# Performance work log

Measured on AMD Instinct MI355X. Metric: run time of the kernel, lower is better.

The kernel has to match this reference:

```python
import jax, jax.numpy as jnp
import numpy as np

N_HEAD = 12
D_MODEL = 768
B, T = 1, 1024


def _rope(x):
    # x: (B, H, T, Dh). Matches torch RoPE: split even/odd, cat halves.
    Dh = x.shape[-1]
    t = x.shape[2]
    inv_freq = 1.0 / (10000.0 ** (jnp.arange(0, Dh, 2, dtype=jnp.float32) / Dh))
    freqs = jnp.arange(t, dtype=jnp.float32)[:, None] * inv_freq[None, :]  # (T, Dh/2)
    cos = jnp.cos(freqs)[None, None]  # (1,1,T,Dh/2)
    sin = jnp.sin(freqs)[None, None]
    x1 = x[..., 0::2]
    x2 = x[..., 1::2]
    return jnp.concatenate([-x2 * sin + x1 * cos, x1 * sin + x2 * cos], axis=-1)


def _wedge(x, A, id_bias):
    # S = (A - A^T) + diag(id_bias_h), per head h; x: (B,H,T,Dh)
    skew = A - A.T  # (Dh, Dh)
    S = skew[None, :, :] + jax.vmap(jnp.diag)(id_bias)  # (H, Dh, Dh)
    flow = jnp.einsum('bhtd,hde->bhte', x, S)
    return x + flow


def _forward(x, WV_w, WV_b, WK_w, WK_b, WQ_w, A, id_bias, sink, v_nulls, WO_w, WO_b):
    b, t, c = x.shape
    n_br = WO_w.shape[0]
    n_sh = n_br
    dh = c // n_br
    h_tot = n_br * n_sh
    scale = dh ** -0.5

    q = (x @ WQ_w).reshape(b, t, h_tot, dh).transpose(0, 2, 1, 3)      # (B,Htot,T,Dh)
    k_base = (x @ WK_w + WK_b).reshape(b, t, n_sh, dh).transpose(0, 2, 1, 3)
    v_base = (x @ WV_w + WV_b).reshape(b, t, n_sh, dh).transpose(0, 2, 1, 3)
    k = jnp.tile(k_base, (1, n_br, 1, 1))  # (B,Htot,T,Dh)
    v = jnp.tile(v_base, (1, n_br, 1, 1))

    q = _rope(_wedge(q, A, id_bias))
    k = _rope(_wedge(k, A, id_bias))

    scores = jnp.einsum('bhtd,bhsd->bhts', q, k) * scale  # (B,Htot,T,T)
    causal = jnp.tril(jnp.ones((t, t), dtype=bool))
    scores = jnp.where(causal[None, None], scores, -jnp.inf)

    sinks = jnp.broadcast_to(sink.reshape(1, h_tot, 1, 1), (b, h_tot, t, 1))
    probs = jax.nn.softmax(jnp.concatenate([scores, sinks], axis=-1), axis=-1)
    probs_tok, probs_sink = probs[..., :t], probs[..., t:]

    out_tok = jnp.einsum('bhts,bhsd->bhtd', probs_tok, v)
    out_sink = probs_sink * v_nulls.reshape(h_tot, dh)[None, :, None, :]
    ctx = out_tok + out_sink  # (B,Htot,T,Dh)

    ctx = ctx.reshape(b, n_br, n_sh, t, dh).transpose(0, 1, 3, 2, 4).reshape(b, n_br, t, c)
    y = jnp.einsum('bntc,ncd->bntd', ctx, WO_w) + WO_b[None, :, None, :]
    return y.mean(axis=1)  # (B,T,C)


def setup_inputs() -> dict:
    key = jax.random.key(0)
    ks = jax.random.split(key, 12)
    c = D_MODEL
    n_br = N_HEAD
    dh = c // n_br
    h_tot = n_br * n_br
    s = 0.02
    return {
        'x': jax.random.normal(ks[0], (B, T, c), dtype=jnp.float32),
        'WV_w': jax.random.normal(ks[1], (c, c), dtype=jnp.float32) * s,
        'WV_b': jnp.zeros((c,), dtype=jnp.float32),
        'WK_w': jax.random.normal(ks[2], (c, c), dtype=jnp.float32) * s,
        'WK_b': jnp.zeros((c,), dtype=jnp.float32),
        'WQ_w': jax.random.normal(ks[3], (c, c * n_br), dtype=jnp.float32) * s,
        'A': jax.random.normal(ks[4], (dh, dh), dtype=jnp.float32) * s,
        'id_bias': jax.random.normal(ks[5], (h_tot, dh), dtype=jnp.float32) * s,
        'sink': jax.random.normal(ks[6], (h_tot,), dtype=jnp.float32) * s,
        'v_nulls': jax.random.normal(ks[7], (n_br, c), dtype=jnp.float32) * s,
        'WO_w': jax.random.normal(ks[8], (n_br, c, c), dtype=jnp.float32) * (1.0 / np.sqrt(c)),
        'WO_b': jnp.zeros((n_br, c), dtype=jnp.float32),
    }


def reference(x, WV_w, WV_b, WK_w, WK_b, WQ_w, A, id_bias, sink, v_nulls, WO_w, WO_b):
    return _forward(x, WV_w, WV_b, WK_w, WK_b, WQ_w, A, id_bias, sink, v_nulls, WO_w, WO_b)
```

## Files before the change

### kernel.cpp

```cpp
#include <hip/hip_runtime.h>
#include <hip/hip_bf16.h>

#define T_SEQ   1024
#define C_MODEL 768
#define N_BR    12
#define DH      64
#define H_TOT   144
#define NQ      9216

typedef __bf16 bf16x8 __attribute__((ext_vector_type(8)));
typedef float  f32x4  __attribute__((ext_vector_type(4)));
typedef unsigned int u32x4 __attribute__((ext_vector_type(4)));
typedef unsigned short u16;

#define SM_OFF 3.0f
#define LOG2E  1.44269504089f
#define QSCALE (0.125f * LOG2E)

__device__ __forceinline__ void gload16(void* lds, const void* g)
{
    __builtin_amdgcn_global_load_lds(
        (const __attribute__((address_space(1))) void*)g,
        (__attribute__((address_space(3))) void*)lds, 16, 0, 0);
}

__device__ __forceinline__ void split1(float x, u16& h, u16& l)
{
    __bf16 bh = (__bf16)x;
    __bf16 bl = (__bf16)(x - (float)bh);
    h = __builtin_bit_cast(u16, bh);
    l = __builtin_bit_cast(u16, bl);
}

__device__ __forceinline__ u16 tobf(float x)
{
    return __builtin_bit_cast(u16, (__bf16)x);
}

__device__ __forceinline__ unsigned cvtpk(float a, float b)
{
    unsigned r;
    asm("v_cvt_pk_bf16_f32 %0, %1, %2" : "=v"(r) : "v"(a), "v"(b));
    return r;
}

__device__ __forceinline__ float exp2raw(float x)
{
    float r;
    asm("v_exp_f32 %0, %1" : "=v"(r) : "v"(x));
    return r;
}

__device__ __forceinline__ int swb(int row, int byteoff)
{
    return row * 128 + (byteoff ^ ((row & 7) << 4));
}

__device__ __forceinline__ bf16x8 ldsr8(const u16* p, int byteoff)
{
    return *reinterpret_cast<const bf16x8*>(reinterpret_cast<const char*>(p) + byteoff);
}

__device__ __forceinline__ void convt_body(const float* __restrict__ W,
                                           u16* __restrict__ out, int K, int N,
                                           int nx, int ky, float (*t)[33], int tid)
{
    const int n0 = nx * 32;
    const int k0 = ky * 32;
    const int tx = tid & 31;
    const int ty = tid >> 5;
    #pragma unroll
    for (int r = 0; r < 4; ++r)
        t[ty + r * 8][tx] = W[(size_t)(k0 + ty + r * 8) * N + n0 + tx];
    __syncthreads();
    #pragma unroll
    for (int r = 0; r < 4; ++r)
        out[(size_t)(n0 + ty + r * 8) * K + k0 + tx] = tobf(t[tx][ty + r * 8]);
}

__global__ __launch_bounds__(256)
void prep_kernel(const float* __restrict__ x, u16* __restrict__ xh,
                 const float* __restrict__ Amat, const float* __restrict__ id_bias,
                 u16* __restrict__ Mth, u16* __restrict__ Mtl,
                 const float* __restrict__ WO_b, float* __restrict__ mbias,
                 float* __restrict__ tab,
                 const float* __restrict__ WO_w, u16* __restrict__ wot,
                 const float* __restrict__ WK_w, const float* __restrict__ WV_w,
                 u16* __restrict__ wkvt)
{
    __shared__ float tsh[32][33];
    const int b   = blockIdx.x;
    const int tid = threadIdx.x;

    if (b < 128) {
        const int idx = b * 256 + tid;
        const int t = idx >> 5, i = idx & 31;
        const float inv = expf(-(float)i * (logf(10000.f) / 32.f));
        const float fr = (float)t * inv;
        tab[t * 64 + i]      = cosf(fr);
        tab[t * 64 + 32 + i] = sinf(fr);
    } else if (b < 272) {
        const int h = b - 128;
        const int base = tid * 16;
        #pragma unroll
        for (int i = 0; i < 16; ++i) {
            const int idx = base + i;
            const int e = idx >> 6, d = idx & 63;
            float v = Amat[d * 64 + e] - Amat[e * 64 + d];
            if (d == e) v += 1.0f + id_bias[h * 64 + d];
            u16 hh, ll;
            split1(v, hh, ll);
            Mth[(size_t)h * 4096 + idx] = hh;
            Mtl[(size_t)h * 4096 + idx] = ll;
        }
    } else if (b < 275) {
        const int d = (b - 272) * 256 + tid;
        if (d < C_MODEL) {
            float s = 0.f;
            #pragma unroll
            for (int n = 0; n < N_BR; ++n) s += WO_b[n * C_MODEL + d];
            mbias[d] = s * (1.0f / 12.0f);
        }
    } else if (b < 1043) {
        const size_t i = (size_t)(b - 275) * 1024 + tid * 4;
        float4 v = *reinterpret_cast<const float4*>(&x[i]);
        ushort4 o = { tobf(v.x), tobf(v.y), tobf(v.z), tobf(v.w) };
        *reinterpret_cast<ushort4*>(&xh[i]) = o;
    } else if (b < 7955) {
        const int u = b - 1043;
        convt_body(WO_w, wot, NQ, C_MODEL, u % 24, u / 24, tsh, tid);
    } else if (b < 8531) {
        const int u = b - 7955;
        convt_body(WK_w, wkvt, C_MODEL, C_MODEL, u % 24, u / 24, tsh, tid);
    } else {
        const int u = b - 8531;
        convt_body(WV_w, wkvt + 589824, C_MODEL, C_MODEL, u % 24, u / 24, tsh, tid);
    }
}

#define BM 128
#define BN 128
#define BK 32

__global__ __launch_bounds__(256)
void gemm_bf16_kernel(const u16* __restrict__ A, const u16* __restrict__ B,
                      float* __restrict__ Cp, int M, int N, int K)
{
    __shared__ __align__(16) u16 sA[BM * BK], sB[BN * BK];

    const int tid  = threadIdx.x;
    const int lane = tid & 63;
    const int wid  = tid >> 6;
    const int m0   = blockIdx.y * BM;
    const int n0   = blockIdx.x * BN;
    const int kc   = K / gridDim.z;
    const int kbeg = blockIdx.z * kc;
    const int kend = kbeg + kc;

    const int wm = (wid >> 1) * 64;
    const int wn = (wid & 1) * 64;

    f32x4 acc[4][4];
    #pragma unroll
    for (int i = 0; i < 4; ++i)
        #pragma unroll
        for (int j = 0; j < 4; ++j)
            #pragma unroll
            for (int r = 0; r < 4; ++r) acc[i][j][r] = 0.f;

    const int r0 = tid >> 2;
    const int c0 = tid & 3;
    const int rA = wm + (lane & 15);
    const int rB = wn + (lane & 15);
    const int co = (lane >> 4) * 8;

    for (int k0 = kbeg; k0 < kend; k0 += BK) {
        gload16(&sA[(size_t)tid * 8],         &A[(size_t)(m0 + r0)      * K + k0 + c0 * 8]);
        gload16(&sA[(size_t)(tid + 256) * 8], &A[(size_t)(m0 + r0 + 64) * K + k0 + c0 * 8]);
        gload16(&sB[(size_t)tid * 8],         &B[(size_t)(n0 + r0)      * K + k0 + c0 * 8]);
        gload16(&sB[(size_t)(tid + 256) * 8], &B[(size_t)(n0 + r0 + 64) * K + k0 + c0 * 8]);
        __syncthreads();

        bf16x8 ah[4], bh[4];
        #pragma unroll
        for (int i = 0; i < 4; ++i)
            ah[i] = *reinterpret_cast<const bf16x8*>(&sA[(size_t)(rA + i * 16) * BK + co]);
        #pragma unroll
        for (int j = 0; j < 4; ++j)
            bh[j] = *reinterpret_cast<const bf16x8*>(&sB[(size_t)(rB + j * 16) * BK + co]);
        #pragma unroll
        for (int i = 0; i < 4; ++i)
            #pragma unroll
            for (int j = 0; j < 4; ++j)
                acc[i][j] = __builtin_amdgcn_mfma_f32_16x16x32_bf16(ah[i], bh[j], acc[i][j], 0, 0, 0);
        __syncthreads();
    }

    float* Cz = Cp + (size_t)blockIdx.z * M * N;
    const int crow0 = m0 + wm + (lane >> 4) * 4;
    const int ccol0 = n0 + wn + (lane & 15);
    #pragma unroll
    for (int i = 0; i < 4; ++i)
        #pragma unroll
        for (int j = 0; j < 4; ++j)
            #pragma unroll
            for (int r = 0; r < 4; ++r)
                Cz[(size_t)(crow0 + i * 16 + r) * N + ccol0 + j * 16] = acc[i][j][r];
}

__global__ __launch_bounds__(256)
void gemm64_kernel(const u16* __restrict__ A, const u16* __restrict__ B,
                   float* __restrict__ Cp, int M, int N, int K)
{
    __shared__ __align__(16) u16 sA[64 * BK], sB[128 * BK];

    const int tid  = threadIdx.x;
    const int lane = tid & 63;
    const int wid  = tid >> 6;
    const int m0   = blockIdx.y * 64;
    const int n0   = blockIdx.x * 128;
    const int kc   = K / gridDim.z;
    const int kbeg = blockIdx.z * kc;
    const int kend = kbeg + kc;

    const int wm = (wid >> 1) * 32;
    const int wn = (wid & 1) * 64;
    const int g  = lane >> 4;
    const int li = lane & 15;

    f32x4 acc[2][4];
    #pragma unroll
    for (int i = 0; i < 2; ++i)
        #pragma unroll
        for (int j = 0; j < 4; ++j)
            #pragma unroll
            for (int r = 0; r < 4; ++r) acc[i][j][r] = 0.f;

    const int r0 = tid >> 2;
    const int c0 = (tid & 3) * 8;

    for (int k0 = kbeg; k0 < kend; k0 += BK) {
        gload16(&sA[(size_t)tid * 8],         &A[(size_t)(m0 + r0)      * K + k0 + c0]);
        gload16(&sB[(size_t)tid * 8],         &B[(size_t)(n0 + r0)      * K + k0 + c0]);
        gload16(&sB[(size_t)(tid + 256) * 8], &B[(size_t)(n0 + r0 + 64) * K + k0 + c0]);
        __syncthreads();

        bf16x8 ah[2], bh[4];
        #pragma unroll
        for (int i = 0; i < 2; ++i)
            ah[i] = *reinterpret_cast<const bf16x8*>(&sA[(size_t)(wm + 16 * i + li) * BK + g * 8]);
        #pragma unroll
        for (int j = 0; j < 4; ++j)
            bh[j] = *reinterpret_cast<const bf16x8*>(&sB[(size_t)(wn + 16 * j + li) * BK + g * 8]);
        #pragma unroll
        for (int i = 0; i < 2; ++i)
            #pragma unroll
            for (int j = 0; j < 4; ++j)
                acc[i][j] = __builtin_amdgcn_mfma_f32_16x16x32_bf16(ah[i], bh[j], acc[i][j], 0, 0, 0);
        __syncthreads();
    }

    float* Cz = Cp + (size_t)blockIdx.z * M * N;
    const int crow0 = m0 + wm + g * 4;
    const int ccol0 = n0 + wn + li;
    #pragma unroll
    for (int i = 0; i < 2; ++i)
        #pragma unroll
        for (int j = 0; j < 4; ++j)
            #pragma unroll
            for (int r = 0; r < 4; ++r)
                Cz[(size_t)(crow0 + i * 16 + r) * N + ccol0 + j * 16] = acc[i][j][r];
}

__global__ __launch_bounds__(256)
void gemm_q_rope_kernel(const u16* __restrict__ A, const u16* __restrict__ B,
                        const float* __restrict__ tab, u16* __restrict__ Q2)
{
    __shared__ __align__(16) u16 sA[64 * BK], sB[128 * BK];

    const int K = C_MODEL;
    const int tid  = threadIdx.x;
    const int lane = tid & 63;
    const int wid  = tid >> 6;
    const int m0   = blockIdx.y * 64;
    const int n0   = blockIdx.x * 128;

    const int wm = (wid >> 1) * 32;
    const int wn = (wid & 1) * 64;
    const int g  = lane >> 4;
    const int li = lane & 15;

    f32x4 acc[2][4];
    #pragma unroll
    for (int i = 0; i < 2; ++i)
        #pragma unroll
        for (int j = 0; j < 4; ++j)
            #pragma unroll
            for (int r = 0; r < 4; ++r) acc[i][j][r] = 0.f;

    const int r0 = tid >> 2;
    const int c0 = (tid & 3) * 8;

    for (int k0 = 0; k0 < K; k0 += BK) {
        gload16(&sA[(size_t)tid * 8],         &A[(size_t)(m0 + r0)      * K + k0 + c0]);
        gload16(&sB[(size_t)tid * 8],         &B[(size_t)(n0 + r0)      * K + k0 + c0]);
        gload16(&sB[(size_t)(tid + 256) * 8], &B[(size_t)(n0 + r0 + 64) * K + k0 + c0]);
        __syncthreads();

        bf16x8 ah[2], bh[4];
        #pragma unroll
        for (int i = 0; i < 2; ++i)
            ah[i] = *reinterpret_cast<const bf16x8*>(&sA[(size_t)(wm + 16 * i + li) * BK + g * 8]);
        #pragma unroll
        for (int j = 0; j < 4; ++j)
            bh[j] = *reinterpret_cast<const bf16x8*>(&sB[(size_t)(wn + 16 * j + li) * BK + g * 8]);
        #pragma unroll
        for (int i = 0; i < 2; ++i)
            #pragma unroll
            for (int j = 0; j < 4; ++j)
                acc[i][j] = __builtin_amdgcn_mfma_f32_16x16x32_bf16(ah[i], bh[j], acc[i][j], 0, 0, 0);
        __syncthreads();
    }

    const int h  = (n0 + wn) >> 6;
    const bool ev = (li & 1) == 0;
    #pragma unroll
    for (int j = 0; j < 4; ++j) {
        const int e  = j * 16 + li;
        const int i2 = e >> 1;
        #pragma unroll
        for (int i = 0; i < 2; ++i) {
            #pragma unroll
            for (int r = 0; r < 4; ++r) {
                const int t = m0 + wm + i * 16 + g * 4 + r;
                const float own = acc[i][j][r];
                const float oth = __shfl_xor(own, 1);
                const float cs = tab[t * 64 + i2];
                const float sn = tab[t * 64 + 32 + i2];
                float o; int ch;
                if (ev) { o = own * cs - oth * sn; ch = i2; }
                else    { o = oth * sn + own * cs; ch = 32 + i2; }
                Q2[((size_t)h * T_SEQ + t) * 64 + ch] = tobf(o * QSCALE);
            }
        }
    }
}

__global__ __launch_bounds__(256)
void reduce_kernel(const float* __restrict__ part, float* __restrict__ out,
                   const float* __restrict__ bias, int MN, int N, int Z, float alpha)
{
    const int i = (blockIdx.x * 256 + threadIdx.x) * 4;
    if (i >= MN) return;
    float4 s = *reinterpret_cast<const float4*>(&part[i]);
    for (int z = 1; z < Z; ++z) {
        float4 p = *reinterpret_cast<const float4*>(&part[(size_t)z * MN + i]);
        s.x += p.x; s.y += p.y; s.z += p.z; s.w += p.w;
    }
    s.x *= alpha; s.y *= alpha; s.z *= alpha; s.w *= alpha;
    if (bias) {
        const int c = i % N;
        s.x += bias[c]; s.y += bias[c + 1]; s.z += bias[c + 2]; s.w += bias[c + 3];
    }
    *reinterpret_cast<float4*>(&out[i]) = s;
}

__global__ __launch_bounds__(256)
void reduce_kv_kernel(const float* __restrict__ part, float* __restrict__ out,
                      const float* __restrict__ kb, const float* __restrict__ vb,
                      int MN, int Z)
{
    const int i = (blockIdx.x * 256 + threadIdx.x) * 4;
    if (i >= MN) return;
    float4 s = *reinterpret_cast<const float4*>(&part[i]);
    for (int z = 1; z < Z; ++z) {
        float4 p = *reinterpret_cast<const float4*>(&part[(size_t)z * MN + i]);
        s.x += p.x; s.y += p.y; s.z += p.z; s.w += p.w;
    }
    const int c = i % 1536;
    const float* bp = (c < 768) ? (kb + c) : (vb + c - 768);
    s.x += bp[0]; s.y += bp[1]; s.z += bp[2]; s.w += bp[3];
    *reinterpret_cast<float4*>(&out[i]) = s;
}

__global__ __launch_bounds__(256)
void fold_wq_kernel(const float* __restrict__ WQ, const u16* __restrict__ Mth,
                    const u16* __restrict__ Mtl, u16* __restrict__ wqt)
{
    __shared__ __align__(16) u16 sMh[4096], sMl[4096];
    __shared__ __align__(16) u16 sB[8192];

    const int h   = blockIdx.x;
    const int k0  = blockIdx.y * 128;
    const int tid = threadIdx.x;
    const int lane = tid & 63, w = tid >> 6, g = lane >> 4, li = lane & 15;

    {
        const char* gmh = (const char*)(Mth + (size_t)h * 4096);
        const char* gml = (const char*)(Mtl + (size_t)h * 4096);
        #pragma unroll
        for (int p = 0; p < 2; ++p) {
            const int u = p * 256 + tid;
            const int row = u >> 3, off = (u & 7) * 16;
            const int src = swb(row, off);
            gload16((char*)sMh + u * 16, gmh + src);
            gload16((char*)sMl + u * 16, gml + src);
        }
    }
    {
        const int r    = tid >> 1;
        const int half = tid & 1;
        const float* src = WQ + (size_t)(k0 + r) * NQ + h * 64 + half * 32;
        #pragma unroll
        for (int q = 0; q < 8; ++q) {
            float4 v = *reinterpret_cast<const float4*>(&src[q * 4]);
            ushort4 o = { tobf(v.x), tobf(v.y), tobf(v.z), tobf(v.w) };
            const int byte = swb(r, half * 64 + q * 8);
            *reinterpret_cast<ushort4*>(reinterpret_cast<char*>(sB) + byte) = o;
        }
    }
    __syncthreads();

    f32x4 acc[4][2];
    #pragma unroll
    for (int i = 0; i < 4; ++i)
        #pragma unroll
        for (int jj = 0; jj < 2; ++jj)
            #pragma unroll
            for (int r = 0; r < 4; ++r) acc[i][jj][r] = 0.f;

    bf16x8 ah[4][2], al[4][2];
    #pragma unroll
    for (int i = 0; i < 4; ++i)
        #pragma unroll
        for (int ks = 0; ks < 2; ++ks) {
            ah[i][ks] = ldsr8(sMh, swb(16 * i + li, ks * 64 + g * 16));
            al[i][ks] = ldsr8(sMl, swb(16 * i + li, ks * 64 + g * 16));
        }
    #pragma unroll
    for (int jj = 0; jj < 2; ++jj) {
        const int brow = 16 * (2 * w + jj) + li;
        #pragma unroll
        for (int ks = 0; ks < 2; ++ks) {
            bf16x8 bh = ldsr8(sB, swb(brow, ks * 64 + g * 16));
            #pragma unroll
            for (int i = 0; i < 4; ++i) {
                acc[i][jj] = __builtin_amdgcn_mfma_f32_16x16x32_bf16(ah[i][ks], bh, acc[i][jj], 0, 0, 0);
                acc[i][jj] = __builtin_amdgcn_mfma_f32_16x16x32_bf16(al[i][ks], bh, acc[i][jj], 0, 0, 0);
            }
        }
    }

    #pragma unroll
    for (int i = 0; i < 4; ++i)
        #pragma unroll
        for (int jj = 0; jj < 2; ++jj) {
            const int kc = k0 + 16 * (2 * w + jj) + li;
            #pragma unroll
            for (int r = 0; r < 4; ++r) {
                const int e = 16 * i + g * 4 + r;
                wqt[((size_t)h * 64 + e) * 768 + kc] = tobf(acc[i][jj][r]);
            }
        }
}

__global__ __launch_bounds__(256)
void wedge_vt_kernel(const float* __restrict__ KV, u16* __restrict__ K2,
                     u16* __restrict__ Vt,
                     const u16* __restrict__ Mth, const u16* __restrict__ Mtl,
                     const float* __restrict__ tab)
{
    __shared__ __align__(16) char smem[24576];
    const int b   = blockIdx.x;
    const int t0  = blockIdx.y * 64;
    const int tid = threadIdx.x;

    if (b < H_TOT) {
        u16* sX  = (u16*)smem;
        u16* sMh = (u16*)(smem + 8192);
        u16* sMl = (u16*)(smem + 16384);
        const int h = b;
        const int lane = tid & 63, w = tid >> 6, g = lane >> 4, li = lane & 15;

        {
            const int r  = tid >> 2;
            const int c0 = (tid & 3) * 16;
            const float* xrow = KV + (size_t)(t0 + r) * 1536 + (h % N_BR) * 64;
            #pragma unroll
            for (int q = 0; q < 4; ++q) {
                const int c = c0 + q * 4;
                float4 v = *reinterpret_cast<const float4*>(&xrow[c]);
                ushort4 hv = { tobf(v.x), tobf(v.y), tobf(v.z), tobf(v.w) };
                *reinterpret_cast<ushort4*>((char*)sX + swb(r, 2 * c)) = hv;
            }
        }
        {
            const char* gmh = (const char*)(Mth + (size_t)h * 4096);
            const char* gml = (const char*)(Mtl + (size_t)h * 4096);
            #pragma unroll
            for (int u = 0; u < 2; ++u) {
                const int L = (u * 256 + tid) * 16;
                const int row = L >> 7, off = L & 127;
                const int src = swb(row, off);
                gload16((char*)sMh + L, gmh + src);
                gload16((char*)sMl + L, gml + src);
            }
        }
        __syncthreads();

        f32x4 acc[4];
        #pragma unroll
        for (int j = 0; j < 4; ++j)
            #pragma unroll
            for (int r = 0; r < 4; ++r) acc[j][r] = 0.f;

        bf16x8 ah[2];
        #pragma unroll
        for (int ks = 0; ks < 2; ++ks)
            ah[ks] = ldsr8(sX, swb(w * 16 + li, ks * 64 + g * 16));
        #pragma unroll
        for (int ks = 0; ks < 2; ++ks)
            #pragma unroll
            for (int j = 0; j < 4; ++j) {
                bf16x8 bh = ldsr8(sMh, swb(16 * j + li, ks * 64 + g * 16));
                bf16x8 bl = ldsr8(sMl, swb(16 * j + li, ks * 64 + g * 16));
                acc[j] = __builtin_amdgcn_mfma_f32_16x16x32_bf16(ah[ks], bh, acc[j], 0, 0, 0);
                acc[j] = __builtin_amdgcn_mfma_f32_16x16x32_bf16(ah[ks], bl, acc[j], 0, 0, 0);
            }

        const bool ev = (li & 1) == 0;
        #pragma unroll
        for (int j = 0; j < 4; ++j) {
            const int e = 16 * j + li;
            const int i2 = e >> 1;
            #pragma unroll
            for (int r = 0; r < 4; ++r) {
                const int t = t0 + w * 16 + g * 4 + r;
                const float own = acc[j][r];
                const float oth = __shfl_xor(own, 1);
                const float cs = tab[t * 64 + i2];
                const float sn = tab[t * 64 + 32 + i2];
                float o; int ch;
                if (ev) { o = own * cs - oth * sn; ch = i2; }
                else    { o = oth * sn + own * cs; ch = 32 + i2; }
                K2[((size_t)h * T_SEQ + t) * 64 + ch] = tobf(o);
            }
        }
    } else {
        float (*Ls)[65] = (float (*)[65])smem;
        const int s = b - H_TOT;
        {
            const int r  = tid >> 2;
            const int c0 = (tid & 3) * 16;
            const float* row = KV + (size_t)(t0 + r) * 1536 + 768 + s * 64;
            #pragma unroll
            for (int q = 0; q < 4; ++q) {
                float4 v = *reinterpret_cast<const float4*>(&row[c0 + q * 4]);
                Ls[r][c0 + q * 4 + 0] = v.x; Ls[r][c0 + q * 4 + 1] = v.y;
                Ls[r][c0 + q * 4 + 2] = v.z; Ls[r][c0 + q * 4 + 3] = v.w;
            }
        }
        __syncthreads();
        {
            const int d  = tid >> 2;
            const int tq = (tid & 3) * 16;
            u16* orow = Vt + ((size_t)s * 64 + d) * T_SEQ + t0 + tq;
            #pragma unroll
            for (int q = 0; q < 4; ++q) {
                ushort4 o;
                o.x = tobf(Ls[tq + q * 4 + 0][d]);
                o.y = tobf(Ls[tq + q * 4 + 1][d]);
                o.z = tobf(Ls[tq + q * 4 + 2][d]);
                o.w = tobf(Ls[tq + q * 4 + 3][d]);
                *reinterpret_cast<ushort4*>(&orow[q * 4]) = o;
            }
        }
    }
}

__device__ __forceinline__ void attn_stage_kv(
    int buf, int kv0, int h, int s, int tid,
    const u16* __restrict__ K2, const u16* __restrict__ Vt,
    u16* sK, u16* sV)
{
    const char* gk = (const char*)(K2 + ((size_t)h * T_SEQ + kv0) * 64);
    const char* gv = (const char*)Vt + (size_t)s * 131072 + kv0 * 2;
    #pragma unroll
    for (int p = 0; p < 2; ++p) {
        const int u = p * 256 + tid;
        const int row = u >> 3;
        const int off = (u & 7) * 16;
        const int sw  = off ^ ((row & 7) << 4);
        const int j  = row >> 4, g2 = (row >> 2) & 3, rr = row & 3;
        const int srow = 32 * (j & 1) + 8 * g2 + 4 * (j >> 1) + rr;
        gload16((char*)sK + buf * 8192 + u * 16, gk + srow * 128 + sw);
        gload16((char*)sV + buf * 8192 + u * 16, gv + row * 2048 + sw);
    }
}

template<bool DIAG>
__device__ __forceinline__ void attn_tile_sw(
    int kv0, int qglob, int g, int li,
    const u16* sK, const u16* sV, const bf16x8* qa, const bf16x8 ones,
    f32x4* acc, f32x4& psacc)
{
    f32x4 sacc[4];
    #pragma unroll
    for (int j = 0; j < 4; ++j)
        #pragma unroll
        for (int r = 0; r < 4; ++r) sacc[j][r] = -SM_OFF * LOG2E;

    __builtin_amdgcn_s_setprio(1);
    #pragma unroll
    for (int ks = 0; ks < 2; ++ks)
        #pragma unroll
        for (int j = 0; j < 4; ++j) {
            bf16x8 kb = ldsr8(sK, swb(16 * j + li, ks * 64 + g * 16));
            sacc[j] = __builtin_amdgcn_mfma_f32_16x16x32_bf16(kb, qa[ks], sacc[j], 0, 0, 0);
        }
    __builtin_amdgcn_s_setprio(0);

    float p[4][4];
    const int kvb = kv0 + 8 * g;
    #pragma unroll
    for (int j = 0; j < 4; ++j)
        #pragma unroll
        for (int r = 0; r < 4; ++r) {
            float sv_ = sacc[j][r];
            if (DIAG) {
                const int kv = kvb + 32 * (j & 1) + 4 * (j >> 1) + r;
                if (kv > qglob) sv_ = -__builtin_inff();
            }
            p[j][r] = exp2raw(sv_);
        }

    __builtin_amdgcn_s_setprio(1);
    #pragma unroll
    for (int ks = 0; ks < 2; ++ks) {
        u32x4 pw;
        pw[0] = cvtpk(p[ks][0],     p[ks][1]);
        pw[1] = cvtpk(p[ks][2],     p[ks][3]);
        pw[2] = cvtpk(p[ks + 2][0], p[ks + 2][1]);
        pw[3] = cvtpk(p[ks + 2][2], p[ks + 2][3]);
        bf16x8 pa = __builtin_bit_cast(bf16x8, pw);
        psacc = __builtin_amdgcn_mfma_f32_16x16x32_bf16(ones, pa, psacc, 0, 0, 0);
        #pragma unroll
        for (int j = 0; j < 4; ++j) {
            bf16x8 vb = ldsr8(sV, swb(16 * j + li, ks * 64 + g * 16));
            acc[j] = __builtin_amdgcn_mfma_f32_16x16x32_bf16(vb, pa, acc[j], 0, 0, 0);
        }
    }
    __builtin_amdgcn_s_setprio(0);
}

__global__ __launch_bounds__(256)
void attn_mfma_kernel(const u16* __restrict__ Q2, const u16* __restrict__ K2,
                      const u16* __restrict__ Vt, const float* __restrict__ sink,
                      const float* __restrict__ v_nulls, u16* __restrict__ ctxb)
{
    const int h  = blockIdx.x;
    const int qt = 15 - (int)blockIdx.y;
    const int s  = h % N_BR;
    const int tid  = threadIdx.x;
    const int lane = tid & 63, w = tid >> 6, g = lane >> 4, li = lane & 15;

    __shared__ __align__(16) u16 sK[8192];
    __shared__ __align__(16) u16 sV[8192];

    const u16* qrow = Q2 + ((size_t)h * T_SEQ + qt * 64 + w * 16 + li) * 64;
    bf16x8 qa[2];
    qa[0] = *reinterpret_cast<const bf16x8*>(qrow + g * 8);
    qa[1] = *reinterpret_cast<const bf16x8*>(qrow + 32 + g * 8);

    bf16x8 ones;
    #pragma unroll
    for (int e = 0; e < 8; ++e) ones[e] = (__bf16)1.0f;

    attn_stage_kv(0, 0, h, s, tid, K2, Vt, sK, sV);

    f32x4 acc[4];
    #pragma unroll
    for (int j = 0; j < 4; ++j)
        #pragma unroll
        for (int r = 0; r < 4; ++r) acc[j][r] = 0.f;
    f32x4 psacc;
    #pragma unroll
    for (int r = 0; r < 4; ++r) psacc[r] = 0.f;

    __syncthreads();

    const int qglob = qt * 64 + w * 16 + li;
    const int nt = qt + 1;
    int cur = 0;
    for (int kt = 0; kt < nt - 1; ++kt) {
        attn_stage_kv(cur ^ 1, (kt + 1) * 64, h, s, tid, K2, Vt, sK, sV);
        attn_tile_sw<false>(kt * 64, qglob, g, li,
                            sK + cur * 4096, sV + cur * 4096, qa, ones, acc, psacc);
        __syncthreads();
        cur ^= 1;
    }
    attn_tile_sw<true>(qt * 64, qglob, g, li,
                       sK + cur * 4096, sV + cur * 4096, qa, ones, acc, psacc);

    const float es = __expf(sink[h] - SM_OFF);
    const float rz = 1.0f / (psacc[0] + es);

    const int t = qt * 64 + w * 16 + li;
    u16* orow = ctxb + (size_t)t * NQ + h * 64;
    const float* vn = v_nulls + h * 64;
    #pragma unroll
    for (int j = 0; j < 4; ++j) {
        const int d0 = 16 * j + 4 * g;
        float4 vnv = *reinterpret_cast<const float4*>(&vn[d0]);
        ushort4 o;
        o.x = tobf((acc[j][0] + es * vnv.x) * rz);
        o.y = tobf((acc[j][1] + es * vnv.y) * rz);
        o.z = tobf((acc[j][2] + es * vnv.z) * rz);
        o.w = tobf((acc[j][3] + es * vnv.w) * rz);
        *reinterpret_cast<ushort4*>(&orow[d0]) = o;
    }
}

extern "C" void kernel_launch(void* const* d_in, const int* in_sizes, int n_in,
                              void* d_out, int out_size, void* d_ws, size_t ws_size,
                              hipStream_t stream)
{
    (void)in_sizes; (void)n_in; (void)out_size; (void)ws_size;

    const float* x       = (const float*)d_in[0];
    const float* WV_w    = (const float*)d_in[1];
    const float* WV_b    = (const float*)d_in[2];
    const float* WK_w    = (const float*)d_in[3];
    const float* WK_b    = (const float*)d_in[4];
    const float* WQ_w    = (const float*)d_in[5];
    const float* Amat    = (const float*)d_in[6];
    const float* id_bias = (const float*)d_in[7];
    const float* sink    = (const float*)d_in[8];
    const float* v_nulls = (const float*)d_in[9];
    const float* WO_w    = (const float*)d_in[10];
    const float* WO_b    = (const float*)d_in[11];
    float* out = (float*)d_out;

    float* tab    = (float*)d_ws;
    float* mbias  = tab + 65536;
    float* kvbase = mbias + 768;
    u16* Mth  = (u16*)(kvbase + 1572864);
    u16* Mtl  = Mth + 589824;
    u16* xh   = Mtl + 589824;
    u16* wqt  = xh + 786432;
    u16* wkvt = wqt + 7077888;
    u16* wot  = wkvt + 1179648;
    u16* K2   = wot + 7077888;
    u16* Vt   = K2 + 9437184;
    u16* Q2   = Vt + 786432;
    u16* ctxb = Q2 + 9437184;
    float* pkv = (float*)(ctxb + 9437184);

    float* outpart = (float*)K2;

    const dim3 blk(256);

    prep_kernel<<<dim3(9107), blk, 0, stream>>>(
        x, xh, Amat, id_bias, Mth, Mtl, WO_b, mbias, tab, WO_w, wot, WK_w, WV_w, wkvt);

    fold_wq_kernel<<<dim3(H_TOT, 6), blk, 0, stream>>>(WQ_w, Mth, Mtl, wqt);

    gemm_bf16_kernel<<<dim3(12, 8, 4), blk, 0, stream>>>(
        xh, wkvt, pkv, T_SEQ, 1536, C_MODEL);
    reduce_kv_kernel<<<dim3(1536), blk, 0, stream>>>(pkv, kvbase, WK_b, WV_b, 1572864, 4);

    wedge_vt_kernel<<<dim3(156, 16), blk, 0, stream>>>(
        kvbase, K2, Vt, Mth, Mtl, tab);

    gemm_q_rope_kernel<<<dim3(72, 16), blk, 0, stream>>>(xh, wqt, tab, Q2);

    attn_mfma_kernel<<<dim3(H_TOT, 16), blk, 0, stream>>>(
        Q2, K2, Vt, sink, v_nulls, ctxb);

    gemm64_kernel<<<dim3(6, 16, 12), blk, 0, stream>>>(
        ctxb, wot, outpart, T_SEQ, C_MODEL, NQ);
    reduce_kernel<<<dim3(768), blk, 0, stream>>>(
        outpart, out, mbias, 786432, C_MODEL, 12, 1.0f / 12.0f);
}
```

Baseline: 177.2 us.

## Double-buffer LDS in GEMM kernels, add XCD-aware block swizzle, shrink split-K

The three GEMM kernels now stage the next K-tile into a second LDS buffer while MFMAs run on the current one, which halves the barriers per iteration and overlaps global loads with compute. Launches switch to 1D grids whose block index is remapped so that consecutive tiles land on the same XCD, aiming for better L2 reuse. The output-projection GEMM drops from 12 to 8 K-splits, cutting partial-sum traffic in the reduce step. The cost is double the LDS per block, which may lower occupancy, and the swizzle relies on the block counts dividing evenly by 8.

After: 167.3 us. 1.06x faster.

```diff
diff --git a/kernel.cpp b/kernel.cpp
--- a/kernel.cpp
+++ b/kernel.cpp
@@ -49,6 +49,11 @@
     float r;
     asm("v_exp_f32 %0, %1" : "=v"(r) : "v"(x));
     return r;
+}
+
+__device__ __forceinline__ int xcd_swz(int bid, int nwg)
+{
+    return (bid & 7) * (nwg >> 3) + (bid >> 3);
 }
 
 __device__ __forceinline__ int swb(int row, int byteoff)
@@ -144,17 +149,24 @@
 
 __global__ __launch_bounds__(256)
 void gemm_bf16_kernel(const u16* __restrict__ A, const u16* __restrict__ B,
-                      float* __restrict__ Cp, int M, int N, int K)
-{
-    __shared__ __align__(16) u16 sA[BM * BK], sB[BN * BK];
+                      float* __restrict__ Cp, int M, int N, int K,
+                      int nx, int ny, int nz)
+{
+    __shared__ __align__(16) u16 sA[2][BM * BK], sB[2][BN * BK];
+
+    const int nwg = nx * ny * nz;
+    const int wg  = xcd_swz(blockIdx.x, nwg);
+    const int x   = wg % nx;
+    const int y   = (wg / nx) % ny;
+    const int z   = wg / (nx * ny);
 
     const int tid  = threadIdx.x;
     const int lane = tid & 63;
     const int wid  = tid >> 6;
-    const int m0   = blockIdx.y * BM;
-    const int n0   = blockIdx.x * BN;
-    const int kc   = K / gridDim.z;
-    const int kbeg = blockIdx.z * kc;
+    const int m0   = y * BM;
+    const int n0   = x * BN;
+    const int kc   = K / nz;
+    const int kbeg = z * kc;
     const int kend = kbeg + kc;
 
     const int wm = (wid >> 1) * 64;
@@ -174,29 +186,36 @@
     const int rB = wn + (lane & 15);
     const int co = (lane >> 4) * 8;
 
+    auto STAGE = [&](int buf, int k0) {
+        gload16(&sA[buf][(size_t)tid * 8],         &A[(size_t)(m0 + r0)      * K + k0 + c0 * 8]);
+        gload16(&sA[buf][(size_t)(tid + 256) * 8], &A[(size_t)(m0 + r0 + 64) * K + k0 + c0 * 8]);
+        gload16(&sB[buf][(size_t)tid * 8],         &B[(size_t)(n0 + r0)      * K + k0 + c0 * 8]);
+        gload16(&sB[buf][(size_t)(tid + 256) * 8], &B[(size_t)(n0 + r0 + 64) * K + k0 + c0 * 8]);
+    };
+
+    STAGE(0, kbeg);
+    __syncthreads();
+    int cur = 0;
     for (int k0 = kbeg; k0 < kend; k0 += BK) {
-        gload16(&sA[(size_t)tid * 8],         &A[(size_t)(m0 + r0)      * K + k0 + c0 * 8]);
-        gload16(&sA[(size_t)(tid + 256) * 8], &A[(size_t)(m0 + r0 + 64) * K + k0 + c0 * 8]);
-        gload16(&sB[(size_t)tid * 8],         &B[(size_t)(n0 + r0)      * K + k0 + c0 * 8]);
-        gload16(&sB[(size_t)(tid + 256) * 8], &B[(size_t)(n0 + r0 + 64) * K + k0 + c0 * 8]);
-        __syncthreads();
+        if (k0 + BK < kend) STAGE(cur ^ 1, k0 + BK);
 
         bf16x8 ah[4], bh[4];
         #pragma unroll
         for (int i = 0; i < 4; ++i)
-            ah[i] = *reinterpret_cast<const bf16x8*>(&sA[(size_t)(rA + i * 16) * BK + co]);
+            ah[i] = *reinterpret_cast<const bf16x8*>(&sA[cur][(size_t)(rA + i * 16) * BK + co]);
         #pragma unroll
         for (int j = 0; j < 4; ++j)
-            bh[j] = *reinterpret_cast<const bf16x8*>(&sB[(size_t)(rB + j * 16) * BK + co]);
+            bh[j] = *reinterpret_cast<const bf16x8*>(&sB[cur][(size_t)(rB + j * 16) * BK + co]);
         #pragma unroll
         for (int i = 0; i < 4; ++i)
             #pragma unroll
             for (int j = 0; j < 4; ++j)
                 acc[i][j] = __builtin_amdgcn_mfma_f32_16x16x32_bf16(ah[i], bh[j], acc[i][j], 0, 0, 0);
         __syncthreads();
-    }
-
-    float* Cz = Cp + (size_t)blockIdx.z * M * N;
+        cur ^= 1;
+    }
+
+    float* Cz = Cp + (size_t)z * M * N;
     const int crow0 = m0 + wm + (lane >> 4) * 4;
     const int ccol0 = n0 + wn + (lane & 15);
     #pragma unroll
@@ -210,17 +229,24 @@
 
 __global__ __launch_bounds__(256)
 void gemm64_kernel(const u16* __restrict__ A, const u16* __restrict__ B,
-                   float* __restrict__ Cp, int M, int N, int K)
-{
-    __shared__ __align__(16) u16 sA[64 * BK], sB[128 * BK];
+                   float* __restrict__ Cp, int M, int N, int K,
+                   int nx, int ny, int nz)
+{
+    __shared__ __align__(16) u16 sA[2][64 * BK], sB[2][128 * BK];
+
+    const int nwg = nx * ny * nz;
+    const int wg  = xcd_swz(blockIdx.x, nwg);
+    const int x   = wg % nx;
+    const int y   = (wg / nx) % ny;
+    const int z   = wg / (nx * ny);
 
     const int tid  = threadIdx.x;
     const int lane = tid & 63;
     const int wid  = tid >> 6;
-    const int m0   = blockIdx.y * 64;
-    const int n0   = blockIdx.x * 128;
-    const int kc   = K / gridDim.z;
-    const int kbeg = blockIdx.z * kc;
+    const int m0   = y * 64;
+    const int n0   = x * 128;
+    const int kc   = K / nz;
+    const int kbeg = z * kc;
     const int kend = kbeg + kc;
 
     const int wm = (wid >> 1) * 32;
@@ -239,28 +265,35 @@
     const int r0 = tid >> 2;
     const int c0 = (tid & 3) * 8;
 
+    auto STAGE = [&](int buf, int k0) {
+        gload16(&sA[buf][(size_t)tid * 8],         &A[(size_t)(m0 + r0)      * K + k0 + c0]);
+        gload16(&sB[buf][(size_t)tid * 8],         &B[(size_t)(n0 + r0)      * K + k0 + c0]);
+        gload16(&sB[buf][(size_t)(tid + 256) * 8], &B[(size_t)(n0 + r0 + 64) * K + k0 + c0]);
+    };
+
+    STAGE(0, kbeg);
+    __syncthreads();
+    int cur = 0;
     for (int k0 = kbeg; k0 < kend; k0 += BK) {
-        gload16(&sA[(size_t)tid * 8],         &A[(size_t)(m0 + r0)      * K + k0 + c0]);
-        gload16(&sB[(size_t)tid * 8],         &B[(size_t)(n0 + r0)      * K + k0 + c0]);
-        gload16(&sB[(size_t)(tid + 256) * 8], &B[(size_t)(n0 + r0 + 64) * K + k0 + c0]);
-        __syncthreads();
+        if (k0 + BK < kend) STAGE(cur ^ 1, k0 + BK);
 
         bf16x8 ah[2], bh[4];
         #pragma unroll
         for (int i = 0; i < 2; ++i)
-            ah[i] = *reinterpret_cast<const bf16x8*>(&sA[(size_t)(wm + 16 * i + li) * BK + g * 8]);
+            ah[i] = *reinterpret_cast<const bf16x8*>(&sA[cur][(size_t)(wm + 16 * i + li) * BK + g * 8]);
         #pragma unroll
         for (int j = 0; j < 4; ++j)
-            bh[j] = *reinterpret_cast<const bf16x8*>(&sB[(size_t)(wn + 16 * j + li) * BK + g * 8]);
+            bh[j] = *reinterpret_cast<const bf16x8*>(&sB[cur][(size_t)(wn + 16 * j + li) * BK + g * 8]);
         #pragma unroll
         for (int i = 0; i < 2; ++i)
             #pragma unroll
             for (int j = 0; j < 4; ++j)
                 acc[i][j] = __builtin_amdgcn_mfma_f32_16x16x32_bf16(ah[i], bh[j], acc[i][j], 0, 0, 0);
         __syncthreads();
-    }
-
-    float* Cz = Cp + (size_t)blockIdx.z * M * N;
+        cur ^= 1;
+    }
+
+    float* Cz = Cp + (size_t)z * M * N;
     const int crow0 = m0 + wm + g * 4;
     const int ccol0 = n0 + wn + li;
     #pragma unroll
@@ -276,14 +309,18 @@
 void gemm_q_rope_kernel(const u16* __restrict__ A, const u16* __restrict__ B,
                         const float* __restrict__ tab, u16* __restrict__ Q2)
 {
-    __shared__ __align__(16) u16 sA[64 * BK], sB[128 * BK];
+    __shared__ __align__(16) u16 sA[2][64 * BK], sB[2][128 * BK];
 
     const int K = C_MODEL;
+    const int wg = xcd_swz(blockIdx.x, 1152);
+    const int y  = wg & 15;
+    const int x  = wg >> 4;
+
     const int tid  = threadIdx.x;
     const int lane = tid & 63;
     const int wid  = tid >> 6;
-    const int m0   = blockIdx.y * 64;
-    const int n0   = blockIdx.x * 128;
+    const int m0   = y * 64;
+    const int n0   = x * 128;
 
     const int wm = (wid >> 1) * 32;
     const int wn = (wid & 1) * 64;
@@ -301,25 +338,32 @@
     const int r0 = tid >> 2;
     const int c0 = (tid & 3) * 8;
 
+    auto STAGE = [&](int buf, int k0) {
+        gload16(&sA[buf][(size_t)tid * 8],         &A[(size_t)(m0 + r0)      * K + k0 + c0]);
+        gload16(&sB[buf][(size_t)tid * 8],         &B[(size_t)(n0 + r0)      * K + k0 + c0]);
+        gload16(&sB[buf][(size_t)(tid + 256) * 8], &B[(size_t)(n0 + r0 + 64) * K + k0 + c0]);
+    };
+
+    STAGE(0, 0);
+    __syncthreads();
+    int cur = 0;
     for (int k0 = 0; k0 < K; k0 += BK) {
-        gload16(&sA[(size_t)tid * 8],         &A[(size_t)(m0 + r0)      * K + k0 + c0]);
-        gload16(&sB[(size_t)tid * 8],         &B[(size_t)(n0 + r0)      * K + k0 + c0]);
-        gload16(&sB[(size_t)(tid + 256) * 8], &B[(size_t)(n0 + r0 + 64) * K + k0 + c0]);
-        __syncthreads();
+        if (k0 + BK < K) STAGE(cur ^ 1, k0 + BK);
 
         bf16x8 ah[2], bh[4];
         #pragma unroll
         for (int i = 0; i < 2; ++i)
-            ah[i] = *reinterpret_cast<const bf16x8*>(&sA[(size_t)(wm + 16 * i + li) * BK + g * 8]);
+            ah[i] = *reinterpret_cast<const bf16x8*>(&sA[cur][(size_t)(wm + 16 * i + li) * BK + g * 8]);
         #pragma unroll
         for (int j = 0; j < 4; ++j)
-            bh[j] = *reinterpret_cast<const bf16x8*>(&sB[(size_t)(wn + 16 * j + li) * BK + g * 8]);
+            bh[j] = *reinterpret_cast<const bf16x8*>(&sB[cur][(size_t)(wn + 16 * j + li) * BK + g * 8]);
         #pragma unroll
         for (int i = 0; i < 2; ++i)
             #pragma unroll
             for (int j = 0; j < 4; ++j)
                 acc[i][j] = __builtin_amdgcn_mfma_f32_16x16x32_bf16(ah[i], bh[j], acc[i][j], 0, 0, 0);
         __syncthreads();
+        cur ^= 1;
     }
 
     const int h  = (n0 + wn) >> 6;
@@ -765,20 +809,20 @@
 
     fold_wq_kernel<<<dim3(H_TOT, 6), blk, 0, stream>>>(WQ_w, Mth, Mtl, wqt);
 
-    gemm_bf16_kernel<<<dim3(12, 8, 4), blk, 0, stream>>>(
-        xh, wkvt, pkv, T_SEQ, 1536, C_MODEL);
+    gemm_bf16_kernel<<<dim3(384), blk, 0, stream>>>(
+        xh, wkvt, pkv, T_SEQ, 1536, C_MODEL, 12, 8, 4);
     reduce_kv_kernel<<<dim3(1536), blk, 0, stream>>>(pkv, kvbase, WK_b, WV_b, 1572864, 4);
 
     wedge_vt_kernel<<<dim3(156, 16), blk, 0, stream>>>(
         kvbase, K2, Vt, Mth, Mtl, tab);
 
-    gemm_q_rope_kernel<<<dim3(72, 16), blk, 0, stream>>>(xh, wqt, tab, Q2);
+    gemm_q_rope_kernel<<<dim3(1152), blk, 0, stream>>>(xh, wqt, tab, Q2);
 
     attn_mfma_kernel<<<dim3(H_TOT, 16), blk, 0, stream>>>(
         Q2, K2, Vt, sink, v_nulls, ctxb);
 
-    gemm64_kernel<<<dim3(6, 16, 12), blk, 0, stream>>>(
-        ctxb, wot, outpart, T_SEQ, C_MODEL, NQ);
+    gemm64_kernel<<<dim3(768), blk, 0, stream>>>(
+        ctxb, wot, outpart, T_SEQ, C_MODEL, NQ, 6, 16, 8);
     reduce_kernel<<<dim3(768), blk, 0, stream>>>(
-        outpart, out, mbias, 786432, C_MODEL, 12, 1.0f / 12.0f);
-}
+        outpart, out, mbias, 786432, C_MODEL, 8, 1.0f / 12.0f);
+}
```
